# Optimization experiments

Hardware: AMD Instinct MI355X
Metric: run time of the kernel (lower is better)

## Reference

```python
import jax, jax.numpy as jnp
import numpy as np

H = 256       # hidden_dim
E = H // 2    # operator embedding dim
T = 12        # num_tempers
O = 3         # num_ops per temper
HOPS = 4      # max_path_hops
B = 128       # batch
D = 2048      # input_dim
NCLS = 10     # task_head classes


def setup_inputs() -> dict:
    key = jax.random.key(0)
    ks = jax.random.split(key, 12)
    x = jax.random.normal(ks[0], (B, D), jnp.float32)
    N = B * (D // H)  # 1024 patch tokens
    # per-hop routed temper per patch; value == T means halt
    sampled_tempers = jax.random.randint(ks[1], (HOPS, N), 0, T + 1, jnp.int32)
    sampled_ops = jax.random.randint(ks[2], (HOPS, N), 0, O, jnp.int32)
    s1 = 1.0 / np.sqrt(H + E)
    W1 = jax.random.uniform(ks[3], (T, O, H + E, H), jnp.float32, -s1, s1)
    b1 = jax.random.uniform(ks[4], (T, O, H), jnp.float32, -s1, s1)
    s2 = 1.0 / np.sqrt(H)
    W2 = jax.random.uniform(ks[5], (T, O, H, H), jnp.float32, -s2, s2)
    b2 = jax.random.uniform(ks[6], (T, O, H), jnp.float32, -s2, s2)
    op_emb = jax.random.normal(ks[7], (T, O, E), jnp.float32)
    ln_g = jnp.ones((H,), jnp.float32)
    ln_b = jnp.zeros((H,), jnp.float32)
    Wt = jax.random.uniform(ks[8], (H, NCLS), jnp.float32, -s2, s2)
    bt = jax.random.uniform(ks[9], (NCLS,), jnp.float32, -s2, s2)
    return dict(x=x, W1=W1, b1=b1, W2=W2, b2=b2, op_emb=op_emb,
                ln_g=ln_g, ln_b=ln_b, Wt=Wt, bt=bt,
                sampled_tempers=sampled_tempers, sampled_ops=sampled_ops)


def reference(x, W1, b1, W2, b2, op_emb, ln_g, ln_b, Wt, bt,
              sampled_tempers, sampled_ops):
    Bsz, Din = x.shape
    pad = (-Din) % H
    if pad > 0:
        x = jnp.pad(x, ((0, 0), (0, pad)))
    state = x.reshape(-1, H)                       # [N, H] patch states
    active = jnp.ones((state.shape[0],), bool)     # not-yet-halted mask
    for hop in range(HOPS):
        t = sampled_tempers[hop]
        o = sampled_ops[hop]
        active = active & (t != T)                 # T == halt action
        tc = jnp.clip(t, 0, T - 1)                 # safe index for halted rows
        emb = op_emb[tc, o]                        # [N, E] op embedding gather
        xa = jnp.concatenate([state, emb], axis=-1)  # [N, H+E]
        # per-token expert weight gather + batched matvec (memory-bound dispatch)
        h = jax.nn.relu(jnp.einsum('ni,nio->no', xa, W1[tc, o]) + b1[tc, o])
        y = jax.nn.relu(jnp.einsum('ni,nio->no', h, W2[tc, o]) + b2[tc, o])
        state = jnp.where(active[:, None], y, state)
    pooled = state.reshape(Bsz, -1, H).mean(axis=1)   # [B, H]
    mu = pooled.mean(axis=-1, keepdims=True)
    var = pooled.var(axis=-1, keepdims=True)
    normed = (pooled - mu) * jax.lax.rsqrt(var + 1e-5) * ln_g + ln_b
    return normed @ Wt + bt                           # [B, 10]
```

## Files before the change

### kernel.cpp

```cpp
#include <hip/hip_runtime.h>

typedef __attribute__((ext_vector_type(8))) short short8;
typedef __attribute__((ext_vector_type(4))) float floatx4;

#define NEXP   36
#define NTOK   1024
#define HOPS   4

#define OFF_STATE   0u
#define OFF_W1B     1048576u
#define OFF_W2B     5767168u
#define OFF_C1      10485760u
#define OFF_COUNTS  10522624u
#define OFF_LISTS   10523264u
#define OFF_JOBS    11113088u
#define OFF_NJ      11115136u

__device__ __forceinline__ unsigned short f2bf(float f) {
    unsigned u = __float_as_uint(f);
    u += 0x7FFFu + ((u >> 16) & 1u);
    return (unsigned short)(u >> 16);
}

__global__ __launch_bounds__(256) void prep_kernel(
    const float* __restrict__ W1, const float* __restrict__ b1,
    const float* __restrict__ W2, const float* __restrict__ op_emb,
    const int* __restrict__ tempers, const int* __restrict__ ops,
    unsigned short* __restrict__ W1b, unsigned short* __restrict__ W2b,
    float* __restrict__ c1, int* __restrict__ counts, int* __restrict__ lists,
    int* __restrict__ jobs, int* __restrict__ njobs)
{
    const int bid = blockIdx.x;
    const int t = threadIdx.x;

    if (bid < 2304) {
        const int mat = bid / 1152;
        const int id  = bid % 1152;
        const int e   = id / 32;
        const int sub = id % 32;
        const int kb  = sub / 4;
        const int jt  = sub % 4;
        const float* src = mat ? (W2 + e * 65536) : (W1 + e * 98304);
        unsigned short* dst = (mat ? W2b : W1b) + e * 65536;
        const int j  = jt * 64 + (t & 63);
        const int ks = (t >> 6) * 8;
        short8 v;
        #pragma unroll
        for (int i = 0; i < 8; i++)
            v[i] = (short)f2bf(src[(kb * 32 + ks + i) * 256 + j]);
        *(short8*)(dst + (kb * 256 + j) * 32 + ks) = v;
    } else if (bid < 2340) {
        const int e = bid - 2304;
        __shared__ float eb[128];
        if (t < 128) eb[t] = op_emb[e * 128 + t];
        __syncthreads();
        float acc = b1[e * 256 + t];
        const float* wp = W1 + e * 98304 + 256 * 256;
        #pragma unroll 4
        for (int k = 0; k < 128; k++)
            acc += eb[k] * wp[k * 256 + t];
        c1[e * 256 + t] = acc;
    } else {
        __shared__ int lc[HOPS * NEXP];
        if (t < HOPS * NEXP) lc[t] = 0;
        __syncthreads();
        for (int q = 0; q < 4; q++) {
            int n = q * 256 + t;
            bool act = true;
            for (int hop = 0; hop < HOPS; hop++) {
                int tt = tempers[hop * NTOK + n];
                int oo = ops[hop * NTOK + n];
                act = act && (tt != 12);
                if (act) {
                    int e = tt * 3 + oo;
                    int pos = atomicAdd(&lc[hop * NEXP + e], 1);
                    lists[(hop * NEXP + e) * NTOK + pos] = n;
                }
            }
        }
        __syncthreads();
        if (t < HOPS * NEXP) counts[t] = lc[t];
        if (t < HOPS) {
            int hop = t, nj = 0;
            for (int e = 0; e < NEXP; e++) {
                int c = lc[hop * NEXP + e];
                for (int m0 = 0; m0 < c; m0 += 16)
                    jobs[hop * 128 + nj++] = (m0 << 8) | e;
            }
            njobs[hop] = nj;
        }
    }
}

__global__ __launch_bounds__(1024, 4) void hop_kernel(
    const float* __restrict__ src, float* __restrict__ state,
    const unsigned short* __restrict__ W1b,
    const unsigned short* __restrict__ W2b,
    const float* __restrict__ c1, const float* __restrict__ b2,
    const int* __restrict__ counts, const int* __restrict__ lists,
    const int* __restrict__ jobs, const int* __restrict__ njobs, int hop)
{
    if (blockIdx.x >= njobs[hop]) return;
    const int job = jobs[hop * 128 + blockIdx.x];
    const int e   = job & 0xFF;
    const int m0  = job >> 8;
    const int n_e = counts[hop * NEXP + e];
    const int mact = min(16, n_e - m0);

    const int t = threadIdx.x;
    const int l = t & 63, w = t >> 6;
    const int col = l & 15, g = l >> 4;
    const int j = w * 16 + col;

    const unsigned short* Wp  = W1b + e * 65536;
    const unsigned short* Wp2 = W2b + e * 65536;
    short8 B1[8], B2[8];
    #pragma unroll
    for (int kb = 0; kb < 8; kb++) {
        B1[kb] = *(const short8*)(Wp  + (kb * 256 + j) * 32 + g * 8);
        B2[kb] = *(const short8*)(Wp2 + (kb * 256 + j) * 32 + g * 8);
    }
    const float cv = c1[e * 256 + j];
    const float bv = b2[e * 256 + j];

    __shared__ int toks[16];
    __shared__ unsigned short Ab[4096];
    __shared__ unsigned short Hb[4096];

    if (t < 16) toks[t] = (t < mact) ? lists[(hop * NEXP + e) * NTOK + m0 + t] : 0;
    __syncthreads();

    {
        int m = t >> 6;
        int k = (t & 63) * 4;
        float4 v = make_float4(0.f, 0.f, 0.f, 0.f);
        if (m < mact) v = *(const float4*)(src + toks[m] * 256 + k);
        int kb = k >> 5, gg = (k >> 3) & 3, i = k & 7;
        unsigned short* d = Ab + kb * 512 + (gg * 16 + m) * 8 + i;
        d[0] = f2bf(v.x); d[1] = f2bf(v.y); d[2] = f2bf(v.z); d[3] = f2bf(v.w);
    }
    __syncthreads();

    floatx4 acc = (floatx4){cv, cv, cv, cv};
    #pragma unroll
    for (int kb = 0; kb < 8; kb++) {
        short8 a = *(const short8*)(Ab + kb * 512 + l * 8);
        acc = __builtin_amdgcn_mfma_f32_16x16x32_bf16(a, B1[kb], acc, 0, 0, 0);
    }
    {
        int kb2 = j >> 5, g2 = (j >> 3) & 3, i2 = j & 7;
        #pragma unroll
        for (int r = 0; r < 4; r++) {
            int m = g * 4 + r;
            float vv = acc[r];
            vv = vv > 0.f ? vv : 0.f;
            Hb[kb2 * 512 + (g2 * 16 + m) * 8 + i2] = f2bf(vv);
        }
    }
    __syncthreads();

    floatx4 acc2 = (floatx4){bv, bv, bv, bv};
    #pragma unroll
    for (int kb = 0; kb < 8; kb++) {
        short8 a = *(const short8*)(Hb + kb * 512 + l * 8);
        acc2 = __builtin_amdgcn_mfma_f32_16x16x32_bf16(a, B2[kb], acc2, 0, 0, 0);
    }
    #pragma unroll
    for (int r = 0; r < 4; r++) {
        int m = g * 4 + r;
        if (m < mact) {
            float vv = acc2[r];
            state[toks[m] * 256 + j] = vv > 0.f ? vv : 0.f;
        }
    }
}

__global__ __launch_bounds__(256) void final_kernel(
    const float* __restrict__ x, const float* __restrict__ state,
    const int* __restrict__ tempers,
    const float* __restrict__ ln_g, const float* __restrict__ ln_b,
    const float* __restrict__ Wt, const float* __restrict__ bt,
    float* __restrict__ out)
{
    const int b = blockIdx.x, t = threadIdx.x;
    float s = 0.f;
    #pragma unroll
    for (int p = 0; p < 8; p++) {
        int n = b * 8 + p;
        const float* rowsrc = (tempers[n] != 12) ? state : x;
        s += rowsrc[n * 256 + t];
    }
    s *= 0.125f;

    float v1 = s, v2 = s * s;
    #pragma unroll
    for (int off = 32; off; off >>= 1) {
        v1 += __shfl_down(v1, off);
        v2 += __shfl_down(v2, off);
    }
    __shared__ float red[8];
    __shared__ float stats[2];
    const int w = t >> 6, l = t & 63;
    if (l == 0) { red[w] = v1; red[4 + w] = v2; }
    __syncthreads();
    if (t == 0) {
        float su = red[0] + red[1] + red[2] + red[3];
        float sq = red[4] + red[5] + red[6] + red[7];
        float mu = su * (1.0f / 256.0f);
        float var = sq * (1.0f / 256.0f) - mu * mu;
        stats[0] = mu;
        stats[1] = rsqrtf(var + 1e-5f);
    }
    __syncthreads();
    float normed = (s - stats[0]) * stats[1] * ln_g[t] + ln_b[t];

    __shared__ float pr[40];
    #pragma unroll
    for (int c = 0; c < 10; c++) {
        float pv = normed * Wt[t * 10 + c];
        #pragma unroll
        for (int off = 32; off; off >>= 1) pv += __shfl_down(pv, off);
        if (l == 0) pr[w * 10 + c] = pv;
    }
    __syncthreads();
    if (t < 10)
        out[b * 10 + t] = pr[t] + pr[10 + t] + pr[20 + t] + pr[30 + t] + bt[t];
}

extern "C" void kernel_launch(void* const* d_in, const int* in_sizes, int n_in,
                              void* d_out, int out_size, void* d_ws, size_t ws_size,
                              hipStream_t stream)
{
    const float* x      = (const float*)d_in[0];
    const float* W1     = (const float*)d_in[1];
    const float* b1     = (const float*)d_in[2];
    const float* W2     = (const float*)d_in[3];
    const float* b2     = (const float*)d_in[4];
    const float* op_emb = (const float*)d_in[5];
    const float* ln_g   = (const float*)d_in[6];
    const float* ln_b   = (const float*)d_in[7];
    const float* Wt     = (const float*)d_in[8];
    const float* bt     = (const float*)d_in[9];
    const int* tempers  = (const int*)d_in[10];
    const int* ops      = (const int*)d_in[11];

    char* ws = (char*)d_ws;
    float* state          = (float*)(ws + OFF_STATE);
    unsigned short* W1b   = (unsigned short*)(ws + OFF_W1B);
    unsigned short* W2b   = (unsigned short*)(ws + OFF_W2B);
    float* c1             = (float*)(ws + OFF_C1);
    int* counts           = (int*)(ws + OFF_COUNTS);
    int* lists            = (int*)(ws + OFF_LISTS);
    int* jobs             = (int*)(ws + OFF_JOBS);
    int* njobs            = (int*)(ws + OFF_NJ);
    float* out            = (float*)d_out;

    prep_kernel<<<2341, 256, 0, stream>>>(W1, b1, W2, op_emb, tempers, ops,
                                          W1b, W2b, c1, counts, lists,
                                          jobs, njobs);
    for (int hop = 0; hop < HOPS; hop++)
        hop_kernel<<<128, 1024, 0, stream>>>(hop == 0 ? x : state, state,
                                             W1b, W2b, c1, b2,
                                             counts, lists, jobs, njobs, hop);
    final_kernel<<<128, 256, 0, stream>>>(x, state, tempers,
                                          ln_g, ln_b, Wt, bt, out);
}
```

Before: 141.4 us.

## Fuse prep, hop and final kernels into one cooperative persistent kernel

Replaces six kernel launches with one cooperative launch of 256 blocks that use grid syncs between phases. Each expert is pinned to one block, which keeps that expert's bf16 weight fragments in registers across all four hops and loops over that expert's token tiles serially, rather than spreading tiles over blocks. The aim is to remove launch gaps and repeated weight loads. The cost is that only 36 blocks do the hop work, so busy experts become serial, and grid.sync adds its own overhead.

```diff
diff --git a/kernel.cpp b/kernel.cpp
--- a/kernel.cpp
+++ b/kernel.cpp
@@ -1,4 +1,7 @@
 #include <hip/hip_runtime.h>
+#include <hip/hip_cooperative_groups.h>
+
+namespace cg = cooperative_groups;
 
 typedef __attribute__((ext_vector_type(8))) short short8;
 typedef __attribute__((ext_vector_type(4))) float floatx4;
@@ -6,6 +9,7 @@
 #define NEXP   36
 #define NTOK   1024
 #define HOPS   4
+#define NBLK   256
 
 #define OFF_STATE   0u
 #define OFF_W1B     1048576u
@@ -13,8 +17,6 @@
 #define OFF_C1      10485760u
 #define OFF_COUNTS  10522624u
 #define OFF_LISTS   10523264u
-#define OFF_JOBS    11113088u
-#define OFF_NJ      11115136u
 
 __device__ __forceinline__ unsigned short f2bf(float f) {
     unsigned u = __float_as_uint(f);
@@ -22,209 +24,209 @@
     return (unsigned short)(u >> 16);
 }
 
-__global__ __launch_bounds__(256) void prep_kernel(
-    const float* __restrict__ W1, const float* __restrict__ b1,
-    const float* __restrict__ W2, const float* __restrict__ op_emb,
+__global__ __launch_bounds__(1024, 4) void fused_kernel(
+    const float* __restrict__ x, const float* __restrict__ W1,
+    const float* __restrict__ b1, const float* __restrict__ W2,
+    const float* __restrict__ b2, const float* __restrict__ op_emb,
+    const float* __restrict__ ln_g, const float* __restrict__ ln_b,
+    const float* __restrict__ Wt, const float* __restrict__ bt,
     const int* __restrict__ tempers, const int* __restrict__ ops,
     unsigned short* __restrict__ W1b, unsigned short* __restrict__ W2b,
     float* __restrict__ c1, int* __restrict__ counts, int* __restrict__ lists,
-    int* __restrict__ jobs, int* __restrict__ njobs)
+    float* __restrict__ state, float* __restrict__ out)
 {
+    cg::grid_group grid = cg::this_grid();
     const int bid = blockIdx.x;
-    const int t = threadIdx.x;
-
-    if (bid < 2304) {
-        const int mat = bid / 1152;
-        const int id  = bid % 1152;
-        const int e   = id / 32;
-        const int sub = id % 32;
-        const int kb  = sub / 4;
-        const int jt  = sub % 4;
-        const float* src = mat ? (W2 + e * 65536) : (W1 + e * 98304);
-        unsigned short* dst = (mat ? W2b : W1b) + e * 65536;
-        const int j  = jt * 64 + (t & 63);
-        const int ks = (t >> 6) * 8;
-        short8 v;
-        #pragma unroll
-        for (int i = 0; i < 8; i++)
-            v[i] = (short)f2bf(src[(kb * 32 + ks + i) * 256 + j]);
-        *(short8*)(dst + (kb * 256 + j) * 32 + ks) = v;
-    } else if (bid < 2340) {
-        const int e = bid - 2304;
-        __shared__ float eb[128];
-        if (t < 128) eb[t] = op_emb[e * 128 + t];
-        __syncthreads();
-        float acc = b1[e * 256 + t];
-        const float* wp = W1 + e * 98304 + 256 * 256;
-        #pragma unroll 4
-        for (int k = 0; k < 128; k++)
-            acc += eb[k] * wp[k * 256 + t];
-        c1[e * 256 + t] = acc;
-    } else {
-        __shared__ int lc[HOPS * NEXP];
-        if (t < HOPS * NEXP) lc[t] = 0;
-        __syncthreads();
-        for (int q = 0; q < 4; q++) {
-            int n = q * 256 + t;
-            bool act = true;
-            for (int hop = 0; hop < HOPS; hop++) {
-                int tt = tempers[hop * NTOK + n];
-                int oo = ops[hop * NTOK + n];
-                act = act && (tt != 12);
-                if (act) {
-                    int e = tt * 3 + oo;
-                    int pos = atomicAdd(&lc[hop * NEXP + e], 1);
-                    lists[(hop * NEXP + e) * NTOK + pos] = n;
-                }
-            }
-        }
-        __syncthreads();
-        if (t < HOPS * NEXP) counts[t] = lc[t];
-        if (t < HOPS) {
-            int hop = t, nj = 0;
-            for (int e = 0; e < NEXP; e++) {
-                int c = lc[hop * NEXP + e];
-                for (int m0 = 0; m0 < c; m0 += 16)
-                    jobs[hop * 128 + nj++] = (m0 << 8) | e;
-            }
-            njobs[hop] = nj;
-        }
-    }
-}
-
-__global__ __launch_bounds__(1024, 4) void hop_kernel(
-    const float* __restrict__ src, float* __restrict__ state,
-    const unsigned short* __restrict__ W1b,
-    const unsigned short* __restrict__ W2b,
-    const float* __restrict__ c1, const float* __restrict__ b2,
-    const int* __restrict__ counts, const int* __restrict__ lists,
-    const int* __restrict__ jobs, const int* __restrict__ njobs, int hop)
-{
-    if (blockIdx.x >= njobs[hop]) return;
-    const int job = jobs[hop * 128 + blockIdx.x];
-    const int e   = job & 0xFF;
-    const int m0  = job >> 8;
-    const int n_e = counts[hop * NEXP + e];
-    const int mact = min(16, n_e - m0);
-
-    const int t = threadIdx.x;
+    const int t   = threadIdx.x;
+
+    __shared__ unsigned short Ab[4096];
+    __shared__ unsigned short Hb[4096];
+    __shared__ int   toks[16];
+    __shared__ int   lc[HOPS * NEXP];
+    __shared__ float pool[4][256];
+    __shared__ float red[8];
+    __shared__ float stats[2];
+    __shared__ float pr[40];
+
+    for (int task = bid; task < 613; task += NBLK) {
+        if (task == 0) {
+            if (t < HOPS * NEXP) lc[t] = 0;
+            __syncthreads();
+            if (t < 256) {
+                for (int q = 0; q < 4; q++) {
+                    int n = q * 256 + t;
+                    bool act = true;
+                    for (int hop = 0; hop < HOPS; hop++) {
+                        int tt = tempers[hop * NTOK + n];
+                        int oo = ops[hop * NTOK + n];
+                        act = act && (tt != 12);
+                        if (act) {
+                            int eidx = tt * 3 + oo;
+                            int pos = atomicAdd(&lc[hop * NEXP + eidx], 1);
+                            lists[(hop * NEXP + eidx) * NTOK + pos] = n;
+                        }
+                    }
+                }
+            }
+            __syncthreads();
+            if (t < HOPS * NEXP) counts[t] = lc[t];
+        } else if (task <= 36) {
+            const int e = task - 1;
+            if (t < 256) {
+                float acc = b1[e * 256 + t];
+                const float* wp = W1 + e * 98304 + 65536;
+                #pragma unroll 4
+                for (int k = 0; k < 128; k++)
+                    acc += op_emb[e * 128 + k] * wp[k * 256 + t];
+                c1[e * 256 + t] = acc;
+            }
+        } else {
+            const int ct  = task - 37;
+            const int mat = ct / 288;
+            const int id  = ct % 288;
+            const int e   = id / 8;
+            const int kb  = id % 8;
+            const float* src = mat ? (W2 + e * 65536) : (W1 + e * 98304);
+            unsigned short* dst = (mat ? W2b : W1b) + e * 65536;
+            const int j  = (t >> 8) * 64 + (t & 63);
+            const int ks = ((t >> 6) & 3) * 8;
+            short8 v;
+            #pragma unroll
+            for (int i = 0; i < 8; i++)
+                v[i] = (short)f2bf(src[(kb * 32 + ks + i) * 256 + j]);
+            *(short8*)(dst + (kb * 256 + j) * 32 + ks) = v;
+        }
+    }
+    grid.sync();
+
     const int l = t & 63, w = t >> 6;
     const int col = l & 15, g = l >> 4;
     const int j = w * 16 + col;
 
-    const unsigned short* Wp  = W1b + e * 65536;
-    const unsigned short* Wp2 = W2b + e * 65536;
-    short8 B1[8], B2[8];
-    #pragma unroll
-    for (int kb = 0; kb < 8; kb++) {
-        B1[kb] = *(const short8*)(Wp  + (kb * 256 + j) * 32 + g * 8);
-        B2[kb] = *(const short8*)(Wp2 + (kb * 256 + j) * 32 + g * 8);
-    }
-    const float cv = c1[e * 256 + j];
-    const float bv = b2[e * 256 + j];
-
-    __shared__ int toks[16];
-    __shared__ unsigned short Ab[4096];
-    __shared__ unsigned short Hb[4096];
-
-    if (t < 16) toks[t] = (t < mact) ? lists[(hop * NEXP + e) * NTOK + m0 + t] : 0;
-    __syncthreads();
-
-    {
-        int m = t >> 6;
-        int k = (t & 63) * 4;
-        float4 v = make_float4(0.f, 0.f, 0.f, 0.f);
-        if (m < mact) v = *(const float4*)(src + toks[m] * 256 + k);
-        int kb = k >> 5, gg = (k >> 3) & 3, i = k & 7;
-        unsigned short* d = Ab + kb * 512 + (gg * 16 + m) * 8 + i;
-        d[0] = f2bf(v.x); d[1] = f2bf(v.y); d[2] = f2bf(v.z); d[3] = f2bf(v.w);
-    }
-    __syncthreads();
-
-    floatx4 acc = (floatx4){cv, cv, cv, cv};
-    #pragma unroll
-    for (int kb = 0; kb < 8; kb++) {
-        short8 a = *(const short8*)(Ab + kb * 512 + l * 8);
-        acc = __builtin_amdgcn_mfma_f32_16x16x32_bf16(a, B1[kb], acc, 0, 0, 0);
-    }
-    {
-        int kb2 = j >> 5, g2 = (j >> 3) & 3, i2 = j & 7;
+    const int e = bid;
+    short8 B1f[8], B2f[8];
+    float cv = 0.f, bv = 0.f;
+    if (e < NEXP) {
+        const unsigned short* Wp  = W1b + e * 65536;
+        const unsigned short* Wp2 = W2b + e * 65536;
         #pragma unroll
-        for (int r = 0; r < 4; r++) {
-            int m = g * 4 + r;
-            float vv = acc[r];
-            vv = vv > 0.f ? vv : 0.f;
-            Hb[kb2 * 512 + (g2 * 16 + m) * 8 + i2] = f2bf(vv);
-        }
-    }
-    __syncthreads();
-
-    floatx4 acc2 = (floatx4){bv, bv, bv, bv};
-    #pragma unroll
-    for (int kb = 0; kb < 8; kb++) {
-        short8 a = *(const short8*)(Hb + kb * 512 + l * 8);
-        acc2 = __builtin_amdgcn_mfma_f32_16x16x32_bf16(a, B2[kb], acc2, 0, 0, 0);
-    }
-    #pragma unroll
-    for (int r = 0; r < 4; r++) {
-        int m = g * 4 + r;
-        if (m < mact) {
-            float vv = acc2[r];
-            state[toks[m] * 256 + j] = vv > 0.f ? vv : 0.f;
-        }
-    }
-}
-
-__global__ __launch_bounds__(256) void final_kernel(
-    const float* __restrict__ x, const float* __restrict__ state,
-    const int* __restrict__ tempers,
-    const float* __restrict__ ln_g, const float* __restrict__ ln_b,
-    const float* __restrict__ Wt, const float* __restrict__ bt,
-    float* __restrict__ out)
-{
-    const int b = blockIdx.x, t = threadIdx.x;
-    float s = 0.f;
-    #pragma unroll
-    for (int p = 0; p < 8; p++) {
-        int n = b * 8 + p;
-        const float* rowsrc = (tempers[n] != 12) ? state : x;
-        s += rowsrc[n * 256 + t];
-    }
-    s *= 0.125f;
-
-    float v1 = s, v2 = s * s;
-    #pragma unroll
-    for (int off = 32; off; off >>= 1) {
-        v1 += __shfl_down(v1, off);
-        v2 += __shfl_down(v2, off);
-    }
-    __shared__ float red[8];
-    __shared__ float stats[2];
-    const int w = t >> 6, l = t & 63;
-    if (l == 0) { red[w] = v1; red[4 + w] = v2; }
-    __syncthreads();
-    if (t == 0) {
-        float su = red[0] + red[1] + red[2] + red[3];
-        float sq = red[4] + red[5] + red[6] + red[7];
-        float mu = su * (1.0f / 256.0f);
-        float var = sq * (1.0f / 256.0f) - mu * mu;
-        stats[0] = mu;
-        stats[1] = rsqrtf(var + 1e-5f);
-    }
-    __syncthreads();
-    float normed = (s - stats[0]) * stats[1] * ln_g[t] + ln_b[t];
-
-    __shared__ float pr[40];
-    #pragma unroll
-    for (int c = 0; c < 10; c++) {
-        float pv = normed * Wt[t * 10 + c];
-        #pragma unroll
-        for (int off = 32; off; off >>= 1) pv += __shfl_down(pv, off);
-        if (l == 0) pr[w * 10 + c] = pv;
-    }
-    __syncthreads();
-    if (t < 10)
-        out[b * 10 + t] = pr[t] + pr[10 + t] + pr[20 + t] + pr[30 + t] + bt[t];
+        for (int kb = 0; kb < 8; kb++) {
+            B1f[kb] = *(const short8*)(Wp  + (kb * 256 + j) * 32 + g * 8);
+            B2f[kb] = *(const short8*)(Wp2 + (kb * 256 + j) * 32 + g * 8);
+        }
+        cv = c1[e * 256 + j];
+        bv = b2[e * 256 + j];
+    }
+
+    for (int hop = 0; hop < HOPS; hop++) {
+        if (e < NEXP) {
+            const int n_e = counts[hop * NEXP + e];
+            const float* src = hop ? state : x;
+            for (int m0 = 0; m0 < n_e; m0 += 16) {
+                const int mact = min(16, n_e - m0);
+                __syncthreads();
+                if (t < 16)
+                    toks[t] = (t < mact)
+                            ? lists[(hop * NEXP + e) * NTOK + m0 + t] : 0;
+                __syncthreads();
+                {
+                    int m = t >> 6;
+                    int k = (t & 63) * 4;
+                    float4 v = make_float4(0.f, 0.f, 0.f, 0.f);
+                    if (m < mact) v = *(const float4*)(src + toks[m] * 256 + k);
+                    int kb = k >> 5, gg = (k >> 3) & 3, i = k & 7;
+                    unsigned short* d = Ab + kb * 512 + (gg * 16 + m) * 8 + i;
+                    d[0] = f2bf(v.x); d[1] = f2bf(v.y);
+                    d[2] = f2bf(v.z); d[3] = f2bf(v.w);
+                }
+                __syncthreads();
+                floatx4 acc = (floatx4){cv, cv, cv, cv};
+                #pragma unroll
+                for (int kb = 0; kb < 8; kb++) {
+                    short8 a = *(const short8*)(Ab + kb * 512 + l * 8);
+                    acc = __builtin_amdgcn_mfma_f32_16x16x32_bf16(a, B1f[kb], acc, 0, 0, 0);
+                }
+                {
+                    int kb2 = j >> 5, g2 = (j >> 3) & 3, i2 = j & 7;
+                    #pragma unroll
+                    for (int r = 0; r < 4; r++) {
+                        int m = g * 4 + r;
+                        float vv = acc[r];
+                        vv = vv > 0.f ? vv : 0.f;
+                        Hb[kb2 * 512 + (g2 * 16 + m) * 8 + i2] = f2bf(vv);
+                    }
+                }
+                __syncthreads();
+                floatx4 acc2 = (floatx4){bv, bv, bv, bv};
+                #pragma unroll
+                for (int kb = 0; kb < 8; kb++) {
+                    short8 a = *(const short8*)(Hb + kb * 512 + l * 8);
+                    acc2 = __builtin_amdgcn_mfma_f32_16x16x32_bf16(a, B2f[kb], acc2, 0, 0, 0);
+                }
+                #pragma unroll
+                for (int r = 0; r < 4; r++) {
+                    int m = g * 4 + r;
+                    if (m < mact) {
+                        float vv = acc2[r];
+                        state[toks[m] * 256 + j] = vv > 0.f ? vv : 0.f;
+                    }
+                }
+            }
+        }
+        grid.sync();
+    }
+
+    const int b = bid;
+    if (b < 128) {
+        {
+            const int c = t & 255, grp = t >> 8;
+            float s = 0.f;
+            #pragma unroll
+            for (int pp = 0; pp < 2; pp++) {
+                int n = b * 8 + grp * 2 + pp;
+                const float* rowsrc = (tempers[n] != 12) ? state : x;
+                s += rowsrc[n * 256 + c];
+            }
+            pool[grp][c] = s;
+        }
+        __syncthreads();
+        float pooled = 0.f;
+        if (t < 256) {
+            pooled = (pool[0][t] + pool[1][t] + pool[2][t] + pool[3][t]) * 0.125f;
+            float v1 = pooled, v2 = pooled * pooled;
+            #pragma unroll
+            for (int off = 32; off; off >>= 1) {
+                v1 += __shfl_down(v1, off);
+                v2 += __shfl_down(v2, off);
+            }
+            const int wq = t >> 6, lq = t & 63;
+            if (lq == 0) { red[wq] = v1; red[4 + wq] = v2; }
+        }
+        __syncthreads();
+        if (t == 0) {
+            float su = red[0] + red[1] + red[2] + red[3];
+            float sq = red[4] + red[5] + red[6] + red[7];
+            float mu = su * (1.0f / 256.0f);
+            float var = sq * (1.0f / 256.0f) - mu * mu;
+            stats[0] = mu;
+            stats[1] = rsqrtf(var + 1e-5f);
+        }
+        __syncthreads();
+        if (t < 256) {
+            float normed = (pooled - stats[0]) * stats[1] * ln_g[t] + ln_b[t];
+            const int wq = t >> 6, lq = t & 63;
+            #pragma unroll
+            for (int c = 0; c < 10; c++) {
+                float pv = normed * Wt[t * 10 + c];
+                #pragma unroll
+                for (int off = 32; off; off >>= 1) pv += __shfl_down(pv, off);
+                if (lq == 0) pr[wq * 10 + c] = pv;
+            }
+        }
+        __syncthreads();
+        if (t < 10)
+            out[b * 10 + t] = pr[t] + pr[10 + t] + pr[20 + t] + pr[30 + t] + bt[t];
+    }
 }
 
 extern "C" void kernel_launch(void* const* d_in, const int* in_sizes, int n_in,
@@ -251,17 +253,14 @@
     float* c1             = (float*)(ws + OFF_C1);
     int* counts           = (int*)(ws + OFF_COUNTS);
     int* lists            = (int*)(ws + OFF_LISTS);
-    int* jobs             = (int*)(ws + OFF_JOBS);
-    int* njobs            = (int*)(ws + OFF_NJ);
     float* out            = (float*)d_out;
 
-    prep_kernel<<<2341, 256, 0, stream>>>(W1, b1, W2, op_emb, tempers, ops,
-                                          W1b, W2b, c1, counts, lists,
-                                          jobs, njobs);
-    for (int hop = 0; hop < HOPS; hop++)
-        hop_kernel<<<128, 1024, 0, stream>>>(hop == 0 ? x : state, state,
-                                             W1b, W2b, c1, b2,
-                                             counts, lists, jobs, njobs, hop);
-    final_kernel<<<128, 256, 0, stream>>>(x, state, tempers,
-                                          ln_g, ln_b, Wt, bt, out);
+    void* args[] = {
+        (void*)&x, (void*)&W1, (void*)&b1, (void*)&W2, (void*)&b2,
+        (void*)&op_emb, (void*)&ln_g, (void*)&ln_b, (void*)&Wt, (void*)&bt,
+        (void*)&tempers, (void*)&ops, (void*)&W1b, (void*)&W2b, (void*)&c1,
+        (void*)&counts, (void*)&lists, (void*)&state, (void*)&out
+    };
+    hipLaunchCooperativeKernel((void*)fused_kernel, dim3(NBLK), dim3(1024),
+                               args, 0, stream);
 }
```

Result: slower. 292.2 us (+106.6%).

## Replace job list with fixed expert-slot grid and looped token tiles

Applied to the files above, without the earlier changes.

The hop kernel now launches a fixed 40x4 grid indexed by expert and slot instead of reading a prep-built job table. Each block loops over token tiles with stride 64, so its register-resident expert weights are reused across several tiles. The single-thread serial job-building loop in prep is dropped. Prep weight-conversion blocks are renumbered so consecutive block IDs spread across experts, presumably to balance memory channels. The change adds per-tile barriers, and experts with more than 64 tokens are now handled serially inside one block.

```diff
diff --git a/kernel.cpp b/kernel.cpp
--- a/kernel.cpp
+++ b/kernel.cpp
@@ -13,8 +13,6 @@
 #define OFF_C1      10485760u
 #define OFF_COUNTS  10522624u
 #define OFF_LISTS   10523264u
-#define OFF_JOBS    11113088u
-#define OFF_NJ      11115136u
 
 __device__ __forceinline__ unsigned short f2bf(float f) {
     unsigned u = __float_as_uint(f);
@@ -27,19 +25,21 @@
     const float* __restrict__ W2, const float* __restrict__ op_emb,
     const int* __restrict__ tempers, const int* __restrict__ ops,
     unsigned short* __restrict__ W1b, unsigned short* __restrict__ W2b,
-    float* __restrict__ c1, int* __restrict__ counts, int* __restrict__ lists,
-    int* __restrict__ jobs, int* __restrict__ njobs)
+    float* __restrict__ c1, int* __restrict__ counts, int* __restrict__ lists)
 {
     const int bid = blockIdx.x;
     const int t = threadIdx.x;
 
-    if (bid < 2304) {
-        const int mat = bid / 1152;
-        const int id  = bid % 1152;
-        const int e   = id / 32;
-        const int sub = id % 32;
-        const int kb  = sub / 4;
-        const int jt  = sub % 4;
+    if (bid < 2880) {
+        const int r  = bid & 7;
+        const int q  = bid >> 3;
+        const int e  = r + 8 * (q >> 6);
+        if (e >= NEXP) return;
+        const int sub = q & 63;
+        const int mat = sub >> 5;
+        const int s2  = sub & 31;
+        const int kb  = s2 >> 2;
+        const int jt  = s2 & 3;
         const float* src = mat ? (W2 + e * 65536) : (W1 + e * 98304);
         unsigned short* dst = (mat ? W2b : W1b) + e * 65536;
         const int j  = jt * 64 + (t & 63);
@@ -49,13 +49,13 @@
         for (int i = 0; i < 8; i++)
             v[i] = (short)f2bf(src[(kb * 32 + ks + i) * 256 + j]);
         *(short8*)(dst + (kb * 256 + j) * 32 + ks) = v;
-    } else if (bid < 2340) {
-        const int e = bid - 2304;
+    } else if (bid < 2916) {
+        const int e = bid - 2880;
         __shared__ float eb[128];
         if (t < 128) eb[t] = op_emb[e * 128 + t];
         __syncthreads();
         float acc = b1[e * 256 + t];
-        const float* wp = W1 + e * 98304 + 256 * 256;
+        const float* wp = W1 + e * 98304 + 65536;
         #pragma unroll 4
         for (int k = 0; k < 128; k++)
             acc += eb[k] * wp[k * 256 + t];
@@ -80,15 +80,6 @@
         }
         __syncthreads();
         if (t < HOPS * NEXP) counts[t] = lc[t];
-        if (t < HOPS) {
-            int hop = t, nj = 0;
-            for (int e = 0; e < NEXP; e++) {
-                int c = lc[hop * NEXP + e];
-                for (int m0 = 0; m0 < c; m0 += 16)
-                    jobs[hop * 128 + nj++] = (m0 << 8) | e;
-            }
-            njobs[hop] = nj;
-        }
     }
 }
 
@@ -97,15 +88,13 @@
     const unsigned short* __restrict__ W1b,
     const unsigned short* __restrict__ W2b,
     const float* __restrict__ c1, const float* __restrict__ b2,
-    const int* __restrict__ counts, const int* __restrict__ lists,
-    const int* __restrict__ jobs, const int* __restrict__ njobs, int hop)
-{
-    if (blockIdx.x >= njobs[hop]) return;
-    const int job = jobs[hop * 128 + blockIdx.x];
-    const int e   = job & 0xFF;
-    const int m0  = job >> 8;
+    const int* __restrict__ counts, const int* __restrict__ lists, int hop)
+{
+    const int e    = blockIdx.x % 40;
+    const int slot = blockIdx.x / 40;
+    if (e >= NEXP) return;
     const int n_e = counts[hop * NEXP + e];
-    const int mact = min(16, n_e - m0);
+    if (slot * 16 >= n_e) return;
 
     const int t = threadIdx.x;
     const int l = t & 63, w = t >> 6;
@@ -120,6 +109,11 @@
         B1[kb] = *(const short8*)(Wp  + (kb * 256 + j) * 32 + g * 8);
         B2[kb] = *(const short8*)(Wp2 + (kb * 256 + j) * 32 + g * 8);
     }
+    #pragma unroll
+    for (int kb = 0; kb < 8; kb++) {
+        asm volatile("" : "+v"(B1[kb]));
+        asm volatile("" : "+v"(B2[kb]));
+    }
     const float cv = c1[e * 256 + j];
     const float bv = b2[e * 256 + j];
 
@@ -127,50 +121,55 @@
     __shared__ unsigned short Ab[4096];
     __shared__ unsigned short Hb[4096];
 
-    if (t < 16) toks[t] = (t < mact) ? lists[(hop * NEXP + e) * NTOK + m0 + t] : 0;
-    __syncthreads();
-
-    {
-        int m = t >> 6;
-        int k = (t & 63) * 4;
-        float4 v = make_float4(0.f, 0.f, 0.f, 0.f);
-        if (m < mact) v = *(const float4*)(src + toks[m] * 256 + k);
-        int kb = k >> 5, gg = (k >> 3) & 3, i = k & 7;
-        unsigned short* d = Ab + kb * 512 + (gg * 16 + m) * 8 + i;
-        d[0] = f2bf(v.x); d[1] = f2bf(v.y); d[2] = f2bf(v.z); d[3] = f2bf(v.w);
-    }
-    __syncthreads();
-
-    floatx4 acc = (floatx4){cv, cv, cv, cv};
-    #pragma unroll
-    for (int kb = 0; kb < 8; kb++) {
-        short8 a = *(const short8*)(Ab + kb * 512 + l * 8);
-        acc = __builtin_amdgcn_mfma_f32_16x16x32_bf16(a, B1[kb], acc, 0, 0, 0);
-    }
-    {
-        int kb2 = j >> 5, g2 = (j >> 3) & 3, i2 = j & 7;
+    for (int m0 = slot * 16; m0 < n_e; m0 += 64) {
+        const int mact = min(16, n_e - m0);
+        __syncthreads();
+        if (t < 16)
+            toks[t] = (t < mact) ? lists[(hop * NEXP + e) * NTOK + m0 + t] : 0;
+        __syncthreads();
+
+        {
+            int m = t >> 6;
+            int k = (t & 63) * 4;
+            float4 v = make_float4(0.f, 0.f, 0.f, 0.f);
+            if (m < mact) v = *(const float4*)(src + toks[m] * 256 + k);
+            int kb = k >> 5, gg = (k >> 3) & 3, i = k & 7;
+            unsigned short* d = Ab + kb * 512 + (gg * 16 + m) * 8 + i;
+            d[0] = f2bf(v.x); d[1] = f2bf(v.y); d[2] = f2bf(v.z); d[3] = f2bf(v.w);
+        }
+        __syncthreads();
+
+        floatx4 acc = (floatx4){cv, cv, cv, cv};
+        #pragma unroll
+        for (int kb = 0; kb < 8; kb++) {
+            short8 a = *(const short8*)(Ab + kb * 512 + l * 8);
+            acc = __builtin_amdgcn_mfma_f32_16x16x32_bf16(a, B1[kb], acc, 0, 0, 0);
+        }
+        {
+            int kb2 = j >> 5, g2 = (j >> 3) & 3, i2 = j & 7;
+            #pragma unroll
+            for (int r = 0; r < 4; r++) {
+                int m = g * 4 + r;
+                float vv = acc[r];
+                vv = vv > 0.f ? vv : 0.f;
+                Hb[kb2 * 512 + (g2 * 16 + m) * 8 + i2] = f2bf(vv);
+            }
+        }
+        __syncthreads();
+
+        floatx4 acc2 = (floatx4){bv, bv, bv, bv};
+        #pragma unroll
+        for (int kb = 0; kb < 8; kb++) {
+            short8 a = *(const short8*)(Hb + kb * 512 + l * 8);
+            acc2 = __builtin_amdgcn_mfma_f32_16x16x32_bf16(a, B2[kb], acc2, 0, 0, 0);
+        }
         #pragma unroll
         for (int r = 0; r < 4; r++) {
             int m = g * 4 + r;
-            float vv = acc[r];
-            vv = vv > 0.f ? vv : 0.f;
-            Hb[kb2 * 512 + (g2 * 16 + m) * 8 + i2] = f2bf(vv);
-        }
-    }
-    __syncthreads();
-
-    floatx4 acc2 = (floatx4){bv, bv, bv, bv};
-    #pragma unroll
-    for (int kb = 0; kb < 8; kb++) {
-        short8 a = *(const short8*)(Hb + kb * 512 + l * 8);
-        acc2 = __builtin_amdgcn_mfma_f32_16x16x32_bf16(a, B2[kb], acc2, 0, 0, 0);
-    }
-    #pragma unroll
-    for (int r = 0; r < 4; r++) {
-        int m = g * 4 + r;
-        if (m < mact) {
-            float vv = acc2[r];
-            state[toks[m] * 256 + j] = vv > 0.f ? vv : 0.f;
+            if (m < mact) {
+                float vv = acc2[r];
+                state[toks[m] * 256 + j] = vv > 0.f ? vv : 0.f;
+            }
         }
     }
 }
@@ -251,17 +250,14 @@
     float* c1             = (float*)(ws + OFF_C1);
     int* counts           = (int*)(ws + OFF_COUNTS);
     int* lists            = (int*)(ws + OFF_LISTS);
-    int* jobs             = (int*)(ws + OFF_JOBS);
-    int* njobs            = (int*)(ws + OFF_NJ);
     float* out            = (float*)d_out;
 
-    prep_kernel<<<2341, 256, 0, stream>>>(W1, b1, W2, op_emb, tempers, ops,
-                                          W1b, W2b, c1, counts, lists,
-                                          jobs, njobs);
+    prep_kernel<<<2917, 256, 0, stream>>>(W1, b1, W2, op_emb, tempers, ops,
+                                          W1b, W2b, c1, counts, lists);
     for (int hop = 0; hop < HOPS; hop++)
-        hop_kernel<<<128, 1024, 0, stream>>>(hop == 0 ? x : state, state,
+        hop_kernel<<<160, 1024, 0, stream>>>(hop == 0 ? x : state, state,
                                              W1b, W2b, c1, b2,
-                                             counts, lists, jobs, njobs, hop);
+                                             counts, lists, hop);
     final_kernel<<<128, 256, 0, stream>>>(x, state, tempers,
                                           ln_g, ln_b, Wt, bt, out);
 }
```

After: 138.1 us. 1.02x faster.
